# Performance work log

Measured on AMD Instinct MI355X. Metric: run time of the kernel, lower is better.

Reference implementation:

```python
import jax, jax.numpy as jnp
import numpy as np

N_POINTS = 1_000_000
NUM_SEGMENTS = 100_000
D_IN = 64
FEA_COMPRE = 16  # linear: 64 -> 2*fea_compre = 32


def setup_inputs() -> dict:
    key = jax.random.key(0)
    k1, k2, k3, k4, k5 = jax.random.split(key, 5)
    shuffled_ind = jax.random.permutation(k1, N_POINTS)  # shuffle of point rows
    pt_gfeatures = jax.random.normal(k2, (N_POINTS, D_IN), dtype=jnp.float32)
    pt_localfeatures2 = jax.random.normal(k3, (N_POINTS, D_IN), dtype=jnp.float32)
    pt_inv = jnp.sort(jax.random.randint(k4, (N_POINTS,), 0, NUM_SEGMENTS))
    W = jax.random.normal(k5, (D_IN, 2 * FEA_COMPRE), dtype=jnp.float32) * (1.0 / np.sqrt(D_IN))
    b = jnp.zeros((2 * FEA_COMPRE,), dtype=jnp.float32)
    return {
        "shuffled_ind": shuffled_ind,
        "pt_gfeatures": pt_gfeatures,
        "pt_localfeatures2": pt_localfeatures2,
        "pt_inv": pt_inv,
        "W": W,
        "b": b,
    }


def reference(shuffled_ind, pt_gfeatures, pt_localfeatures2, pt_inv, W, b):
    # gather + add fused expression: [N, 64]
    x = pt_gfeatures[shuffled_ind, :] + pt_localfeatures2
    # scatter_max over segments: [M, 64]
    pooled = jax.ops.segment_max(x, pt_inv, num_segments=NUM_SEGMENTS)
    # empty segments come back as -inf; torch_scatter leaves them at fill value -> use 0
    pooled = jnp.where(jnp.isfinite(pooled), pooled, jnp.zeros((), pooled.dtype))
    # fea_compre*2 = 32 is in (0, 64), so the compression branch runs
    return jax.nn.relu(pooled @ W + b)  # [M, 32]
```

## Files before the change

kernel.cpp:

```cpp
#include <hip/hip_runtime.h>
#include <hip/hip_bf16.h>
#include <math.h>


#define D_IN 64
#define K_OUT 32
#define RPW 128
#define WPB 4
#define ENC_NEG_INF 0x007FFFFFu

__device__ __forceinline__ unsigned enc_f32(float f) {
    unsigned u = __float_as_uint(f);
    return (u & 0x80000000u) ? ~u : (u | 0x80000000u);
}
__device__ __forceinline__ float dec_f32(unsigned u) {
    unsigned b = (u & 0x80000000u) ? (u ^ 0x80000000u) : ~u;
    return __uint_as_float(b);
}

__global__ __launch_bounds__(256) void init_pooled_kernel(uint4* __restrict__ p, int n4)
{
    const uint4 v = make_uint4(ENC_NEG_INF, ENC_NEG_INF, ENC_NEG_INF, ENC_NEG_INF);
    for (int i = blockIdx.x * blockDim.x + threadIdx.x; i < n4; i += gridDim.x * blockDim.x)
        p[i] = v;
}

__global__ __launch_bounds__(64 * WPB) void scan_max_kernel(
    const int*   __restrict__ shuffled_ind,
    const float* __restrict__ g,
    const float* __restrict__ l,
    const int*   __restrict__ pt_inv,
    unsigned*    __restrict__ pooled,
    int n)
{
    __shared__ int ind_lds[WPB][RPW];
    __shared__ int seg_lds[WPB][RPW];

    const int tid  = threadIdx.x;
    const int wid  = tid >> 6;
    const int lane = tid & 63;
    const int rp   = lane >> 4;
    const int cg   = lane & 15;
    const int base = (blockIdx.x * WPB + wid) * RPW;
    const int rows = min(RPW, n - base);

    #pragma unroll
    for (int j0 = 0; j0 < RPW; j0 += 64) {
        const int r = j0 + lane;
        if (r < rows) {
            ind_lds[wid][r] = shuffled_ind[base + r];
            seg_lds[wid][r] = pt_inv[base + r];
        }
    }
    __syncthreads();
    if (rows <= 0) return;

    const int rl      = rows - 1;
    const int ngroups = (rows + 3) >> 2;

    int    curSeg   = seg_lds[wid][0];
    bool   firstRun = true;
    float4 m4 = make_float4(-INFINITY, -INFINITY, -INFINITY, -INFINITY);

    auto load_group = [&](int grp) -> float4 {
        const int irow = min(grp * 4 + rp, rl);
        const int ind  = ind_lds[wid][irow];
        const float4 gv = *reinterpret_cast<const float4*>(g + (size_t)ind * D_IN + cg * 4);
        const float4 lv = *reinterpret_cast<const float4*>(l + (size_t)(base + irow) * D_IN + cg * 4);
        return make_float4(gv.x + lv.x, gv.y + lv.y, gv.z + lv.z, gv.w + lv.w);
    };
    auto acc4 = [&](const float4& x) {
        m4.x = fmaxf(m4.x, x.x); m4.y = fmaxf(m4.y, x.y);
        m4.z = fmaxf(m4.z, x.z); m4.w = fmaxf(m4.w, x.w);
    };
    auto do_flush = [&](int seg, bool useAtomic) {
        float4 t = m4;
        t.x = fmaxf(t.x, __shfl_xor(t.x, 16)); t.y = fmaxf(t.y, __shfl_xor(t.y, 16));
        t.z = fmaxf(t.z, __shfl_xor(t.z, 16)); t.w = fmaxf(t.w, __shfl_xor(t.w, 16));
        t.x = fmaxf(t.x, __shfl_xor(t.x, 32)); t.y = fmaxf(t.y, __shfl_xor(t.y, 32));
        t.z = fmaxf(t.z, __shfl_xor(t.z, 32)); t.w = fmaxf(t.w, __shfl_xor(t.w, 32));
        if (rp == 0) {
            unsigned* p = pooled + (size_t)seg * D_IN + cg * 4;
            const unsigned ex = enc_f32(t.x), ey = enc_f32(t.y),
                           ez = enc_f32(t.z), ew = enc_f32(t.w);
            if (useAtomic) {
                atomicMax(p + 0, ex); atomicMax(p + 1, ey);
                atomicMax(p + 2, ez); atomicMax(p + 3, ew);
            } else {
                *reinterpret_cast<uint4*>(p) = make_uint4(ex, ey, ez, ew);
            }
        }
    };

    float4 xA = load_group(0);
    float4 xB = load_group(1);
    float4 xC = load_group(2);

    for (int grp = 0; grp < ngroups; ++grp) {
        float4 xD = load_group(grp + 3);

        const int i0 = grp * 4;
        const int s3 = seg_lds[wid][min(i0 + 3, rl)];
        if (s3 == curSeg) {
            acc4(xA);
        } else {
            const int s0 = seg_lds[wid][min(i0 + 0, rl)];
            const int s1 = seg_lds[wid][min(i0 + 1, rl)];
            const int s2 = seg_lds[wid][min(i0 + 2, rl)];
            if (s0 != curSeg) { do_flush(curSeg, firstRun); firstRun = false; curSeg = s0;
                                m4 = make_float4(-INFINITY,-INFINITY,-INFINITY,-INFINITY); }
            if (rp == 0) acc4(xA);
            if (s1 != curSeg) { do_flush(curSeg, firstRun); firstRun = false; curSeg = s1;
                                m4 = make_float4(-INFINITY,-INFINITY,-INFINITY,-INFINITY); }
            if (rp == 1) acc4(xA);
            if (s2 != curSeg) { do_flush(curSeg, firstRun); firstRun = false; curSeg = s2;
                                m4 = make_float4(-INFINITY,-INFINITY,-INFINITY,-INFINITY); }
            if (rp == 2) acc4(xA);
            if (s3 != curSeg) { do_flush(curSeg, firstRun); firstRun = false; curSeg = s3;
                                m4 = make_float4(-INFINITY,-INFINITY,-INFINITY,-INFINITY); }
            if (rp == 3) acc4(xA);
        }
        xA = xB; xB = xC; xC = xD;
    }
    do_flush(curSeg, true);
}

__global__ __launch_bounds__(256) void gemm_kernel(
    const unsigned* __restrict__ pooled,
    const float*    __restrict__ W,
    const float*    __restrict__ b,
    float*          __restrict__ out,
    int M)
{
    __shared__ float Ws[D_IN * K_OUT];
    __shared__ float bs[K_OUT];
    __shared__ float pool[WPB][2 * D_IN];

    const int tid = threadIdx.x;
    for (int i = tid; i < D_IN * K_OUT; i += 256) Ws[i] = W[i];
    if (tid < K_OUT) bs[tid] = b[tid];

    const int wid  = tid >> 6;
    const int lane = tid & 63;
    const int s0   = (blockIdx.x * WPB + wid) * 2;

    if (s0 < M) {
        const int nvals = min(2, M - s0) * D_IN;
        uint2 u = make_uint2(ENC_NEG_INF, ENC_NEG_INF);
        if (lane * 2 < nvals)
            u = *reinterpret_cast<const uint2*>(pooled + (size_t)s0 * D_IN + lane * 2);
        pool[wid][lane * 2 + 0] = (u.x == ENC_NEG_INF) ? 0.0f : dec_f32(u.x);
        pool[wid][lane * 2 + 1] = (u.y == ENC_NEG_INF) ? 0.0f : dec_f32(u.y);
    }
    __syncthreads();

    const int h = lane >> 5;
    const int k = lane & 31;
    const int s = s0 + h;
    if (s0 < M && s < M) {
        float acc = bs[k];
        const float* pr = &pool[wid][h * D_IN];
        #pragma unroll
        for (int c = 0; c < D_IN; ++c)
            acc = fmaf(pr[c], Ws[c * K_OUT + k], acc);
        out[(size_t)s * K_OUT + k] = fmaxf(acc, 0.0f);
    }
}

__global__ __launch_bounds__(256) void seg_starts_kernel(
    const int* __restrict__ pt_inv, int n, int* __restrict__ starts, int M)
{
    int s = blockIdx.x * blockDim.x + threadIdx.x;
    if (s > M) return;
    int lo = 0, hi = n;
    while (lo < hi) { int mid = (lo + hi) >> 1; if (pt_inv[mid] < s) lo = mid + 1; else hi = mid; }
    starts[s] = lo;
}

__global__ __launch_bounds__(256) void pool_gemm_kernel(
    const int* __restrict__ shuffled_ind, const float* __restrict__ g,
    const float* __restrict__ l, const int* __restrict__ starts,
    const float* __restrict__ W, const float* __restrict__ b,
    float* __restrict__ out, int M)
{
    __shared__ float Ws[D_IN * K_OUT];
    __shared__ float bs[K_OUT];
    __shared__ float pool[WPB][D_IN];
    const int tid = threadIdx.x;
    for (int i = tid; i < D_IN * K_OUT; i += 256) Ws[i] = W[i];
    if (tid < K_OUT) bs[tid] = b[tid];
    const int wid = tid >> 6, lane = tid & 63;
    const int s = blockIdx.x * WPB + wid;
    const bool active = (s < M);
    float m = -INFINITY;
    if (active) {
        const int p0 = starts[s], p1 = starts[s + 1];
        for (int p = p0; p < p1; ++p) {
            const int ind = shuffled_ind[p];
            m = fmaxf(m, g[(size_t)ind * D_IN + lane] + l[(size_t)p * D_IN + lane]);
        }
        if (p1 <= p0) m = 0.0f;
    }
    if (active) pool[wid][lane] = m;
    __syncthreads();
    if (active && lane < K_OUT) {
        float acc = bs[lane];
        #pragma unroll
        for (int c = 0; c < D_IN; ++c) acc = fmaf(pool[wid][c], Ws[c * K_OUT + lane], acc);
        out[(size_t)s * K_OUT + lane] = fmaxf(acc, 0.0f);
    }
}

extern "C" void kernel_launch(void* const* d_in, const int* in_sizes, int n_in,
                              void* d_out, int out_size, void* d_ws, size_t ws_size,
                              hipStream_t stream)
{
    const int*   shuffled_ind = (const int*)  d_in[0];
    const float* g            = (const float*)d_in[1];
    const float* l            = (const float*)d_in[2];
    const int*   pt_inv       = (const int*)  d_in[3];
    const float* W            = (const float*)d_in[4];
    const float* b            = (const float*)d_in[5];
    float*       out          = (float*)d_out;

    const int N = in_sizes[0];
    const int M = out_size / K_OUT;

    const size_t pooled_bytes = (size_t)M * D_IN * sizeof(unsigned);

    if (ws_size >= pooled_bytes) {
        unsigned* pooled = (unsigned*)d_ws;
        {
            const int n4 = (int)(pooled_bytes / 16);
            init_pooled_kernel<<<512, 256, 0, stream>>>((uint4*)pooled, n4);
        }
        {
            const int rows_per_block = WPB * RPW;
            const int blocks = (N + rows_per_block - 1) / rows_per_block;
            scan_max_kernel<<<blocks, 64 * WPB, 0, stream>>>(
                shuffled_ind, g, l, pt_inv, pooled, N);
        }
        {
            const int blocks = (M + 2 * WPB - 1) / (2 * WPB);
            gemm_kernel<<<blocks, 64 * WPB, 0, stream>>>(pooled, W, b, out, M);
        }
    } else {
        int* starts = (int*)d_ws;
        {
            const int blocks = (M + 1 + 255) / 256;
            seg_starts_kernel<<<blocks, 256, 0, stream>>>(pt_inv, N, starts, M);
        }
        {
            const int blocks = (M + WPB - 1) / WPB;
            pool_gemm_kernel<<<blocks, 64 * WPB, 0, stream>>>(
                shuffled_ind, g, l, starts, W, b, out, M);
        }
    }
}
```

Before: 160.3 us.

## Split scan into per-quarter-wave row strips with register-pipelined vector loads

Replaces the wave-wide scan with one where each 16-lane quarter-wave owns its own 32-row strip. Indices and segment ids are read straight from global memory as int4 instead of being staged through LDS with a block barrier. Gathered and local rows are software-pipelined two chunks ahead in registers, and the cross-quarter shuffle reduction at segment boundaries is removed. In exchange there are more atomicMax flushes per segment, since each strip flushes on its own, and higher register pressure. The fast path is now restricted to N divisible by 4 and at least 8.

```diff
diff --git a/kernel.cpp b/kernel.cpp
--- a/kernel.cpp
+++ b/kernel.cpp
@@ -5,8 +5,10 @@
 
 #define D_IN 64
 #define K_OUT 32
-#define RPW 128
-#define WPB 4
+#define STRIP 32
+#define RPW   128
+#define WPB   4
+#define NCHUNK 8
 #define ENC_NEG_INF 0x007FFFFFu
 
 __device__ __forceinline__ unsigned enc_f32(float f) {
@@ -25,104 +27,114 @@
         p[i] = v;
 }
 
-__global__ __launch_bounds__(64 * WPB) void scan_max_kernel(
-    const int*   __restrict__ shuffled_ind,
+__global__ __launch_bounds__(256) void scan_strip_kernel(
+    const int*   __restrict__ ind_arr,
     const float* __restrict__ g,
     const float* __restrict__ l,
-    const int*   __restrict__ pt_inv,
+    const int*   __restrict__ seg_arr,
     unsigned*    __restrict__ pooled,
     int n)
 {
-    __shared__ int ind_lds[WPB][RPW];
-    __shared__ int seg_lds[WPB][RPW];
-
-    const int tid  = threadIdx.x;
-    const int wid  = tid >> 6;
-    const int lane = tid & 63;
-    const int rp   = lane >> 4;
-    const int cg   = lane & 15;
-    const int base = (blockIdx.x * WPB + wid) * RPW;
-    const int rows = min(RPW, n - base);
-
-    #pragma unroll
-    for (int j0 = 0; j0 < RPW; j0 += 64) {
-        const int r = j0 + lane;
-        if (r < rows) {
-            ind_lds[wid][r] = shuffled_ind[base + r];
-            seg_lds[wid][r] = pt_inv[base + r];
-        }
-    }
-    __syncthreads();
-    if (rows <= 0) return;
-
-    const int rl      = rows - 1;
-    const int ngroups = (rows + 3) >> 2;
-
-    int    curSeg   = seg_lds[wid][0];
+    const int lane  = threadIdx.x & 63;
+    const int wave  = (blockIdx.x * blockDim.x + threadIdx.x) >> 6;
+    const int rp    = lane >> 4;
+    const int cg    = lane & 15;
+    const int sbase = wave * RPW + rp * STRIP;
+    const int nm4   = n - 4;
+    const bool aliveStrip = (sbase < n);
+
+    int4   idq[3], sgq[3];
+    float4 gx[2][4], lx[2][4];
+
+#define CROW(c) (min(sbase + 4*(c), nm4))
+
+    idq[0] = *(const int4*)(ind_arr + CROW(0));
+    sgq[0] = *(const int4*)(seg_arr + CROW(0));
+    idq[1] = *(const int4*)(ind_arr + CROW(1));
+    sgq[1] = *(const int4*)(seg_arr + CROW(1));
+
+    {
+        const size_t rb = (size_t)CROW(0);
+        gx[0][0] = *(const float4*)(g + (size_t)idq[0].x * D_IN + (cg << 2));
+        gx[0][1] = *(const float4*)(g + (size_t)idq[0].y * D_IN + (cg << 2));
+        gx[0][2] = *(const float4*)(g + (size_t)idq[0].z * D_IN + (cg << 2));
+        gx[0][3] = *(const float4*)(g + (size_t)idq[0].w * D_IN + (cg << 2));
+        lx[0][0] = *(const float4*)(l + (rb + 0) * D_IN + (cg << 2));
+        lx[0][1] = *(const float4*)(l + (rb + 1) * D_IN + (cg << 2));
+        lx[0][2] = *(const float4*)(l + (rb + 2) * D_IN + (cg << 2));
+        lx[0][3] = *(const float4*)(l + (rb + 3) * D_IN + (cg << 2));
+    }
+    idq[2] = *(const int4*)(ind_arr + CROW(2));
+    sgq[2] = *(const int4*)(seg_arr + CROW(2));
+    {
+        const size_t rb = (size_t)CROW(1);
+        gx[1][0] = *(const float4*)(g + (size_t)idq[1].x * D_IN + (cg << 2));
+        gx[1][1] = *(const float4*)(g + (size_t)idq[1].y * D_IN + (cg << 2));
+        gx[1][2] = *(const float4*)(g + (size_t)idq[1].z * D_IN + (cg << 2));
+        gx[1][3] = *(const float4*)(g + (size_t)idq[1].w * D_IN + (cg << 2));
+        lx[1][0] = *(const float4*)(l + (rb + 0) * D_IN + (cg << 2));
+        lx[1][1] = *(const float4*)(l + (rb + 1) * D_IN + (cg << 2));
+        lx[1][2] = *(const float4*)(l + (rb + 2) * D_IN + (cg << 2));
+        lx[1][3] = *(const float4*)(l + (rb + 3) * D_IN + (cg << 2));
+    }
+
+    int    curSeg   = sgq[0].x;
     bool   firstRun = true;
     float4 m4 = make_float4(-INFINITY, -INFINITY, -INFINITY, -INFINITY);
 
-    auto load_group = [&](int grp) -> float4 {
-        const int irow = min(grp * 4 + rp, rl);
-        const int ind  = ind_lds[wid][irow];
-        const float4 gv = *reinterpret_cast<const float4*>(g + (size_t)ind * D_IN + cg * 4);
-        const float4 lv = *reinterpret_cast<const float4*>(l + (size_t)(base + irow) * D_IN + cg * 4);
-        return make_float4(gv.x + lv.x, gv.y + lv.y, gv.z + lv.z, gv.w + lv.w);
+    auto flush_run = [&](bool atomic_) {
+        unsigned* p = pooled + (size_t)curSeg * D_IN + (cg << 2);
+        const unsigned e0 = enc_f32(m4.x), e1 = enc_f32(m4.y),
+                       e2 = enc_f32(m4.z), e3 = enc_f32(m4.w);
+        if (atomic_) {
+            atomicMax(p + 0, e0); atomicMax(p + 1, e1);
+            atomicMax(p + 2, e2); atomicMax(p + 3, e3);
+        } else {
+            *reinterpret_cast<uint4*>(p) = make_uint4(e0, e1, e2, e3);
+        }
     };
-    auto acc4 = [&](const float4& x) {
-        m4.x = fmaxf(m4.x, x.x); m4.y = fmaxf(m4.y, x.y);
-        m4.z = fmaxf(m4.z, x.z); m4.w = fmaxf(m4.w, x.w);
+    auto prow = [&](int s, const float4& gv, const float4& lv) {
+        const float4 x = make_float4(gv.x + lv.x, gv.y + lv.y, gv.z + lv.z, gv.w + lv.w);
+        if (s != curSeg) {
+            flush_run(firstRun);
+            firstRun = false;
+            curSeg = s;
+            m4 = x;
+        } else {
+            m4.x = fmaxf(m4.x, x.x); m4.y = fmaxf(m4.y, x.y);
+            m4.z = fmaxf(m4.z, x.z); m4.w = fmaxf(m4.w, x.w);
+        }
     };
-    auto do_flush = [&](int seg, bool useAtomic) {
-        float4 t = m4;
-        t.x = fmaxf(t.x, __shfl_xor(t.x, 16)); t.y = fmaxf(t.y, __shfl_xor(t.y, 16));
-        t.z = fmaxf(t.z, __shfl_xor(t.z, 16)); t.w = fmaxf(t.w, __shfl_xor(t.w, 16));
-        t.x = fmaxf(t.x, __shfl_xor(t.x, 32)); t.y = fmaxf(t.y, __shfl_xor(t.y, 32));
-        t.z = fmaxf(t.z, __shfl_xor(t.z, 32)); t.w = fmaxf(t.w, __shfl_xor(t.w, 32));
-        if (rp == 0) {
-            unsigned* p = pooled + (size_t)seg * D_IN + cg * 4;
-            const unsigned ex = enc_f32(t.x), ey = enc_f32(t.y),
-                           ez = enc_f32(t.z), ew = enc_f32(t.w);
-            if (useAtomic) {
-                atomicMax(p + 0, ex); atomicMax(p + 1, ey);
-                atomicMax(p + 2, ez); atomicMax(p + 3, ew);
-            } else {
-                *reinterpret_cast<uint4*>(p) = make_uint4(ex, ey, ez, ew);
-            }
-        }
-    };
-
-    float4 xA = load_group(0);
-    float4 xB = load_group(1);
-    float4 xC = load_group(2);
-
-    for (int grp = 0; grp < ngroups; ++grp) {
-        float4 xD = load_group(grp + 3);
-
-        const int i0 = grp * 4;
-        const int s3 = seg_lds[wid][min(i0 + 3, rl)];
-        if (s3 == curSeg) {
-            acc4(xA);
-        } else {
-            const int s0 = seg_lds[wid][min(i0 + 0, rl)];
-            const int s1 = seg_lds[wid][min(i0 + 1, rl)];
-            const int s2 = seg_lds[wid][min(i0 + 2, rl)];
-            if (s0 != curSeg) { do_flush(curSeg, firstRun); firstRun = false; curSeg = s0;
-                                m4 = make_float4(-INFINITY,-INFINITY,-INFINITY,-INFINITY); }
-            if (rp == 0) acc4(xA);
-            if (s1 != curSeg) { do_flush(curSeg, firstRun); firstRun = false; curSeg = s1;
-                                m4 = make_float4(-INFINITY,-INFINITY,-INFINITY,-INFINITY); }
-            if (rp == 1) acc4(xA);
-            if (s2 != curSeg) { do_flush(curSeg, firstRun); firstRun = false; curSeg = s2;
-                                m4 = make_float4(-INFINITY,-INFINITY,-INFINITY,-INFINITY); }
-            if (rp == 2) acc4(xA);
-            if (s3 != curSeg) { do_flush(curSeg, firstRun); firstRun = false; curSeg = s3;
-                                m4 = make_float4(-INFINITY,-INFINITY,-INFINITY,-INFINITY); }
-            if (rp == 3) acc4(xA);
-        }
-        xA = xB; xB = xC; xC = xD;
-    }
-    do_flush(curSeg, true);
+
+    #pragma unroll
+    for (int c = 0; c < NCHUNK; ++c) {
+        const int4 sg = sgq[c % 3];
+        const bool alive = (sbase + 4 * c < n);
+        if (alive) {
+            prow(sg.x, gx[c & 1][0], lx[c & 1][0]);
+            prow(sg.y, gx[c & 1][1], lx[c & 1][1]);
+            prow(sg.z, gx[c & 1][2], lx[c & 1][2]);
+            prow(sg.w, gx[c & 1][3], lx[c & 1][3]);
+        }
+        if (c + 3 < NCHUNK) {
+            idq[c % 3] = *(const int4*)(ind_arr + CROW(c + 3));
+            sgq[c % 3] = *(const int4*)(seg_arr + CROW(c + 3));
+        }
+        if (c + 2 < NCHUNK) {
+            const int4 id = idq[(c + 2) % 3];
+            const size_t rb = (size_t)CROW(c + 2);
+            gx[c & 1][0] = *(const float4*)(g + (size_t)id.x * D_IN + (cg << 2));
+            gx[c & 1][1] = *(const float4*)(g + (size_t)id.y * D_IN + (cg << 2));
+            gx[c & 1][2] = *(const float4*)(g + (size_t)id.z * D_IN + (cg << 2));
+            gx[c & 1][3] = *(const float4*)(g + (size_t)id.w * D_IN + (cg << 2));
+            lx[c & 1][0] = *(const float4*)(l + (rb + 0) * D_IN + (cg << 2));
+            lx[c & 1][1] = *(const float4*)(l + (rb + 1) * D_IN + (cg << 2));
+            lx[c & 1][2] = *(const float4*)(l + (rb + 2) * D_IN + (cg << 2));
+            lx[c & 1][3] = *(const float4*)(l + (rb + 3) * D_IN + (cg << 2));
+        }
+    }
+    if (aliveStrip) flush_run(true);
+#undef CROW
 }
 
 __global__ __launch_bounds__(256) void gemm_kernel(
@@ -228,16 +240,16 @@
 
     const size_t pooled_bytes = (size_t)M * D_IN * sizeof(unsigned);
 
-    if (ws_size >= pooled_bytes) {
+    if (ws_size >= pooled_bytes && (N % 4) == 0 && N >= 8) {
         unsigned* pooled = (unsigned*)d_ws;
         {
             const int n4 = (int)(pooled_bytes / 16);
             init_pooled_kernel<<<512, 256, 0, stream>>>((uint4*)pooled, n4);
         }
         {
-            const int rows_per_block = WPB * RPW;
-            const int blocks = (N + rows_per_block - 1) / rows_per_block;
-            scan_max_kernel<<<blocks, 64 * WPB, 0, stream>>>(
+            const int waves  = (N + RPW - 1) / RPW;
+            const int blocks = (waves + WPB - 1) / WPB;
+            scan_strip_kernel<<<blocks, 64 * WPB, 0, stream>>>(
                 shuffled_ind, g, l, pt_inv, pooled, N);
         }
         {
```

Measured after the change: 152.7 us. -4.7%, faster.
